# Optimization experiments

Measured on AMD Instinct MI355X. Metric: run time of the kernel, lower is better.

## Reference

```python
import jax, jax.numpy as jnp
import numpy as np

B, C, L, F = 4096, 1000, 32, 64


def _l2norm(x, eps=1e-12):
    # torch F.normalize: x / max(||x||_2, eps)
    n = jnp.sqrt(jnp.sum(x * x, axis=-1, keepdims=True))
    return x / jnp.maximum(n, eps)


def setup_inputs() -> dict:
    key = jax.random.key(0)
    k1, k2, k3 = jax.random.split(key, 3)
    pe = jax.random.normal(k1, (B, L, F), dtype=jnp.float32)
    cm = jax.random.uniform(k2, (B,), dtype=jnp.float32)
    class_signatures = jax.random.normal(k3, (C, L, F), dtype=jnp.float32) * 0.1
    cantor_prototypes = jnp.linspace(0.0, 1.0, C, dtype=jnp.float32)
    level_resonance = jnp.ones((C, L), dtype=jnp.float32) / L
    return {
        "pe_levels": pe,
        "cantor_measures": cm,
        "class_signatures": class_signatures,
        "cantor_prototypes": cantor_prototypes,
        "level_resonance": level_resonance,
    }


def reference(pe_levels, cantor_measures, class_signatures, cantor_prototypes, level_resonance):
    eps = 1e-6
    # --- triadic compatibility ---
    pe_norm = _l2norm(pe_levels)                     # [B,L,F]
    sig_norm = _l2norm(class_signatures)             # [C,L,F]
    sims = jnp.einsum('blf,clf->bcl', pe_norm, sig_norm)
    sims = (sims + 1.0) * 0.5                        # [B,C,L]
    resonance = jax.nn.softmax(level_resonance, axis=-1)  # [C,L]
    triadic = jnp.sum(sims * resonance[None, :, :], axis=-1)  # [B,C]
    # --- self-similarity pattern (vectorized over level pairs) ---
    a = pe_levels[:, :-1, :]                         # [B,L-1,F]
    b = pe_levels[:, 1:, :]
    cos_eps = 1e-8
    dot = jnp.sum(a * b, axis=-1)
    na = jnp.maximum(jnp.sqrt(jnp.sum(a * a, axis=-1)), cos_eps)
    nb = jnp.maximum(jnp.sqrt(jnp.sum(b * b, axis=-1)), cos_eps)
    self_sim = (dot / (na * nb) + 1.0) * 0.5         # [B,L-1]
    expected = jax.nn.sigmoid(level_resonance[:, :-1] - level_resonance[:, 1:])  # [C,L-1]
    pattern_diff = jnp.abs(self_sim[:, None, :] - expected[None, :, :])  # [B,C,L-1]
    self_sim_compat = jnp.clip(1.0 - jnp.mean(pattern_diff, axis=-1), 0.0, 1.0)  # [B,C]
    # --- cantor compatibility ---
    d = jnp.abs(cantor_measures[:, None] - cantor_prototypes[None, :])
    cantor_compat = jnp.exp(-(d * d) / 0.1) + 1e-8   # [B,C]
    # --- hierarchical compatibility ---
    split = L // 2
    early = _l2norm(jnp.mean(pe_levels[:, :split, :], axis=1))          # [B,F]
    late = _l2norm(jnp.mean(pe_levels[:, split:, :], axis=1))
    early_t = _l2norm(jnp.mean(class_signatures[:, :split, :], axis=1))  # [C,F]
    late_t = _l2norm(jnp.mean(class_signatures[:, split:, :], axis=1))
    early_c = (early @ early_t.T + 1.0) * 0.5
    late_c = (late @ late_t.T + 1.0) * 0.5
    hier = (early_c + late_c) * 0.5                  # [B,C]
    # --- geometric mean of four clamped terms ---
    t = jnp.clip(triadic, eps, 1.0)
    s = jnp.clip(self_sim_compat, eps, 1.0)
    c = jnp.clip(cantor_compat, eps, 1.0)
    h = jnp.clip(hier, eps, 1.0)
    return (t * s * c * h) ** 0.25
```

## Files before the change

kernel.cpp:

```cpp
#include <hip/hip_runtime.h>
#include <hip/hip_bf16.h>
#include <hip/hip_fp8.h>

typedef float f32x4 __attribute__((ext_vector_type(4)));
typedef short bf16x8 __attribute__((ext_vector_type(8)));

#define B_DIM 4096
#define C_DIM 1000
#define CP 1024
#define K1 2048
#define EPS 1e-6f

__device__ __forceinline__ float wsum(float v) {
#pragma unroll
  for (int o = 32; o > 0; o >>= 1) v += __shfl_xor(v, o, 64);
  return v;
}
__device__ __forceinline__ float wmax(float v) {
#pragma unroll
  for (int o = 32; o > 0; o >>= 1) v = fmaxf(v, __shfl_xor(v, o, 64));
  return v;
}

__device__ __forceinline__ void load_lds16(const void* g, void* l) {
  __builtin_amdgcn_global_load_lds(
      (const __attribute__((address_space(1))) unsigned int*)g,
      (__attribute__((address_space(3))) unsigned int*)l, 16, 0, 0);
}

__global__ void prep_all(const float* __restrict__ sig,
                         const float* __restrict__ lr,
                         const float* __restrict__ pe,
                         __hip_fp8_e4m3* __restrict__ wsig,
                         float* __restrict__ expd,
                         __hip_bfloat16* __restrict__ elc,
                         __hip_fp8_e4m3* __restrict__ pen,
                         float* __restrict__ ssb,
                         __hip_bfloat16* __restrict__ elb) {
  __shared__ float LW[4][2304];
  __shared__ float AUX[4][32];
  const int w = threadIdx.x >> 6;
  const int t = threadIdx.x & 63;
  const int unit = blockIdx.x * 4 + w;
  const bool isClass = unit < CP;
  const int c = unit;
  const int b = unit - CP;
  const bool pad = isClass && (c >= C_DIM);
  const float* src = isClass ? (sig + (size_t)c * K1) : (pe + (size_t)b * K1);

#pragma unroll
  for (int i = 0; i < 8; ++i) {
    int o = i * 256 + t * 4;
    f32x4 v = {0.f, 0.f, 0.f, 0.f};
    if (!pad) v = *(const f32x4*)(src + o);
    *(f32x4*)&LW[w][(o >> 6) * 72 + (o & 63)] = v;
  }
  __syncthreads();

  if (isClass) {
    float lv = (t < 32 && !pad) ? lr[c * 32 + t] : -3.0e38f;
    float mx = wmax(lv);
    float ev = (t < 32 && !pad) ? expf(lv - mx) : 0.f;
    float sden = wsum(ev);
    float res = pad ? 0.f : ev / sden;
    float lvn = __shfl_down(lv, 1, 64);
    if (t < 31) {
      expd[c * 32 + t] = pad ? 0.f : 1.f / (1.f + expf(-(lv - lvn)));
    } else if (t == 31) {
      expd[c * 32 + 31] = 0.f;
    }
    if (t < 32) {
      f32x4 sq = {0.f, 0.f, 0.f, 0.f};
#pragma unroll
      for (int i = 0; i < 16; ++i) {
        f32x4 v = *(const f32x4*)&LW[w][t * 72 + i * 4];
        sq += v * v;
      }
      float s = sq[0] + sq[1] + sq[2] + sq[3];
      float inv = 1.f / fmaxf(sqrtf(s), 1e-12f);
      AUX[w][t] = inv * res * 32.f;
    }
  } else {
    if (t < 32) {
      f32x4 sq = {0.f, 0.f, 0.f, 0.f}, dt = {0.f, 0.f, 0.f, 0.f};
      const int tn = (t < 31) ? t + 1 : t;
#pragma unroll
      for (int i = 0; i < 16; ++i) {
        f32x4 v = *(const f32x4*)&LW[w][t * 72 + i * 4];
        f32x4 vn = *(const f32x4*)&LW[w][tn * 72 + i * 4];
        sq += v * v;
        dt += v * vn;
      }
      float s = sq[0] + sq[1] + sq[2] + sq[3];
      float d = dt[0] + dt[1] + dt[2] + dt[3];
      float nrm = sqrtf(s);
      AUX[w][t] = 1.f / fmaxf(nrm, 1e-12f);
      float nn = __shfl_down(nrm, 1, 64);
      if (t < 31)
        ssb[(size_t)b * 32 + t] =
            (d / (fmaxf(nrm, 1e-8f) * fmaxf(nn, 1e-8f)) + 1.f) * 0.5f;
      else
        ssb[(size_t)b * 32 + 31] = 0.f;
    }
  }
  __syncthreads();

  __hip_fp8_e4m3* dst = isClass ? (wsig + (size_t)c * K1) : (pen + (size_t)b * K1);
  float es = 0.f, ls = 0.f;
#pragma unroll
  for (int l = 0; l < 32; ++l) {
    float v = LW[w][l * 72 + t];
    float m = AUX[w][l];
    dst[l * 64 + t] = __hip_fp8_e4m3(v * m);
    if (l < 16) es += v; else ls += v;
  }
  es *= (1.f / 16.f);
  ls *= (1.f / 16.f);
  float en = fmaxf(sqrtf(wsum(es * es)), 1e-12f);
  float ln2 = fmaxf(sqrtf(wsum(ls * ls)), 1e-12f);
  __hip_bfloat16* el = isClass ? (elc + (size_t)c * 128) : (elb + (size_t)b * 128);
  el[t] = __float2bfloat16(es / en);
  el[64 + t] = __float2bfloat16(ls / ln2);
}

__global__ __launch_bounds__(256, 2)
void basin_main(const unsigned char* __restrict__ pen,
                const unsigned char* __restrict__ wsig,
                const __hip_bfloat16* __restrict__ elb,
                const __hip_bfloat16* __restrict__ elc,
                const float* __restrict__ ssb,
                const float* __restrict__ expd,
                const float* __restrict__ cm,
                const float* __restrict__ proto,
                float* __restrict__ out) {
  __shared__ __align__(16) char smem[32768];
  const int t = threadIdx.x;
  const int lane = t & 63;
  const int w = t >> 6;
  const int wm = w >> 1, wn = w & 1;
  const int brow = blockIdx.x * 64;
  const int bcol = blockIdx.y * 64;
  const int srow = t >> 3;
  const int schunk = t & 7;
  const int sel = ((schunk ^ (srow & 7)) << 4);
  const int l15 = lane & 15;
  const int gq = lane >> 4;

  const int rowAb = (wm * 32 + l15) << 7;
  const int rowBb = ((wn * 32 + l15) << 7) + 8192;
  int xg8[4];
#pragma unroll
  for (int kk = 0; kk < 4; ++kk)
    xg8[kk] = ((((kk * 2 + (gq >> 1)) ^ (l15 & 7)) << 4) | ((gq & 1) << 3));
  int xgh[2];
#pragma unroll
  for (int kk = 0; kk < 2; ++kk) xgh[kk] = (((kk * 4 + gq) ^ (l15 & 7)) << 4);

  f32x4 acc1[2][2] = {};
  f32x4 acc2[2][2] = {};

#define STAGE_T(kt, BI)                                                                   \
  do {                                                                                    \
    _Pragma("unroll") for (int i = 0; i < 2; ++i) {                                       \
      load_lds16(pen + (size_t)(brow + i * 32 + srow) * K1 + (kt) * 128 + sel,            \
                 smem + (BI) * 16384 + i * 4096 + t * 16);                                \
      load_lds16(wsig + (size_t)(bcol + i * 32 + srow) * K1 + (kt) * 128 + sel,           \
                 smem + (BI) * 16384 + 8192 + i * 4096 + t * 16);                         \
    }                                                                                     \
  } while (0)

#define STAGE_H(s, BI)                                                                    \
  do {                                                                                    \
    _Pragma("unroll") for (int i = 0; i < 2; ++i) {                                       \
      load_lds16(elb + (size_t)(brow + i * 32 + srow) * 128 + (s) * 64 + (sel >> 1),      \
                 smem + (BI) * 16384 + i * 4096 + t * 16);                                \
      load_lds16(elc + (size_t)(bcol + i * 32 + srow) * 128 + (s) * 64 + (sel >> 1),      \
                 smem + (BI) * 16384 + 8192 + i * 4096 + t * 16);                         \
    }                                                                                     \
  } while (0)

#define COMPUTE(ACC, BI)                                                                  \
  do {                                                                                    \
    _Pragma("unroll") for (int kk = 0; kk < 4; ++kk) {                                    \
      long af[2], bg[2];                                                                  \
      _Pragma("unroll") for (int m = 0; m < 2; ++m)                                       \
          af[m] = *(const long*)(smem + (BI) * 16384 + rowAb + m * 2048 + xg8[kk]);       \
      _Pragma("unroll") for (int n = 0; n < 2; ++n)                                       \
          bg[n] = *(const long*)(smem + (BI) * 16384 + rowBb + n * 2048 + xg8[kk]);       \
      _Pragma("unroll") for (int m = 0; m < 2; ++m)                                       \
        _Pragma("unroll") for (int n = 0; n < 2; ++n)                                     \
          ACC[m][n] = __builtin_amdgcn_mfma_f32_16x16x32_fp8_fp8(af[m], bg[n], ACC[m][n], 0, 0, 0); \
    }                                                                                     \
  } while (0)

#define COMPUTE_H(ACC, BI)                                                                \
  do {                                                                                    \
    _Pragma("unroll") for (int kk = 0; kk < 2; ++kk) {                                    \
      bf16x8 af[2], bg[2];                                                                \
      _Pragma("unroll") for (int m = 0; m < 2; ++m)                                       \
          af[m] = *(const bf16x8*)(smem + (BI) * 16384 + rowAb + m * 2048 + xgh[kk]);     \
      _Pragma("unroll") for (int n = 0; n < 2; ++n)                                       \
          bg[n] = *(const bf16x8*)(smem + (BI) * 16384 + rowBb + n * 2048 + xgh[kk]);     \
      _Pragma("unroll") for (int m = 0; m < 2; ++m)                                       \
        _Pragma("unroll") for (int n = 0; n < 2; ++n)                                     \
          ACC[m][n] = __builtin_amdgcn_mfma_f32_16x16x32_bf16(af[m], bg[n], ACC[m][n], 0, 0, 0); \
    }                                                                                     \
  } while (0)

#define VMW(N) asm volatile("s_waitcnt vmcnt(" #N ")" ::: "memory")
#define BAR()                    \
  __builtin_amdgcn_s_barrier();  \
  __builtin_amdgcn_sched_barrier(0)

#define KSTEP(kt, BI, OTHER)                                                              \
  do {                                                                                    \
    VMW(0);                                                                               \
    BAR();                                                                                \
    if ((kt) + 1 < 16) STAGE_T((kt) + 1, OTHER);                                          \
    COMPUTE(acc1, BI);                                                                    \
  } while (0)

  STAGE_T(0, 0);
  for (int kt = 0; kt < 16; kt += 2) {
    KSTEP(kt, 0, 1);
    KSTEP(kt + 1, 1, 0);
  }
  __syncthreads();

  STAGE_H(0, 0);
  STAGE_H(1, 1);
  VMW(4); BAR();
  COMPUTE_H(acc2, 0);
  VMW(0); BAR();
  COMPUTE_H(acc2, 1);
  __syncthreads();

  float* ss_l = (float*)smem;
  float* ex_l = (float*)(smem + 9216);
  float* cm_l = (float*)(smem + 18432);
  float* pr_l = (float*)(smem + 18688);
  for (int i = t; i < 2048; i += 256) {
    int r = i >> 5, l = i & 31;
    ss_l[r * 36 + l] = ssb[(size_t)(brow + r) * 32 + l];
    ex_l[r * 36 + l] = expd[(size_t)(bcol + r) * 32 + l];
  }
  if (t < 64) cm_l[t] = cm[brow + t];
  else if (t < 128) pr_l[t - 64] = (bcol + t - 64 < C_DIM) ? proto[bcol + t - 64] : 0.f;
  __syncthreads();

  const int col0 = wn * 32 + l15;
  const int row0 = wm * 32 + (gq << 2);
#pragma unroll
  for (int m = 0; m < 2; ++m) {
    float ssum[4][2];
#pragma unroll
    for (int j = 0; j < 4; ++j)
#pragma unroll
      for (int n = 0; n < 2; ++n) ssum[j][n] = 0.f;
#pragma unroll
    for (int l4 = 0; l4 < 32; l4 += 4) {
      f32x4 evv[2], sv[4];
#pragma unroll
      for (int n = 0; n < 2; ++n)
        evv[n] = *(const f32x4*)&ex_l[(col0 + n * 16) * 36 + l4];
#pragma unroll
      for (int j = 0; j < 4; ++j)
        sv[j] = *(const f32x4*)&ss_l[(row0 + m * 16 + j) * 36 + l4];
#pragma unroll
      for (int j = 0; j < 4; ++j)
#pragma unroll
        for (int n = 0; n < 2; ++n) {
          ssum[j][n] += fabsf(sv[j][0] - evv[n][0]) + fabsf(sv[j][1] - evv[n][1]) +
                        fabsf(sv[j][2] - evv[n][2]) + fabsf(sv[j][3] - evv[n][3]);
        }
    }
#pragma unroll
    for (int j = 0; j < 4; ++j) {
      int rloc = row0 + m * 16 + j;
      float cmv = cm_l[rloc];
#pragma unroll
      for (int n = 0; n < 2; ++n) {
        int cloc = col0 + n * 16;
        int cg = bcol + cloc;
        float tria = fminf(fmaxf(0.5f + acc1[m][n][j] * 0.015625f, EPS), 1.0f);
        float hier = fminf(fmaxf(0.5f + 0.25f * acc2[m][n][j], EPS), 1.0f);
        float sc = fminf(fmaxf(1.0f - ssum[j][n] * (1.0f / 31.0f), EPS), 1.0f);
        float d = cmv - pr_l[cloc];
        float cc = __expf(d * d * -10.0f) + 1e-8f;
        cc = fminf(fmaxf(cc, EPS), 1.0f);
        float p = tria * sc * cc * hier;
        if (cg < C_DIM)
          out[(size_t)(brow + rloc) * C_DIM + cg] = sqrtf(sqrtf(p));
      }
    }
  }
}

extern "C" void kernel_launch(void* const* d_in, const int* in_sizes, int n_in,
                              void* d_out, int out_size, void* d_ws, size_t ws_size,
                              hipStream_t stream) {
  (void)in_sizes; (void)n_in; (void)out_size; (void)ws_size;
  const float* pe = (const float*)d_in[0];
  const float* cm = (const float*)d_in[1];
  const float* sig = (const float*)d_in[2];
  const float* proto = (const float*)d_in[3];
  const float* lr = (const float*)d_in[4];
  float* out = (float*)d_out;
  char* ws = (char*)d_ws;

  __hip_fp8_e4m3* wsig = (__hip_fp8_e4m3*)(ws);
  __hip_fp8_e4m3* pen = (__hip_fp8_e4m3*)(ws + 2097152);
  __hip_bfloat16* elb = (__hip_bfloat16*)(ws + 10485760);
  __hip_bfloat16* elc = (__hip_bfloat16*)(ws + 11534336);
  float* ssb = (float*)(ws + 11796480);
  float* expd = (float*)(ws + 12320768);

  prep_all<<<(CP + B_DIM) / 4, 256, 0, stream>>>(sig, lr, pe, wsig, expd, elc, pen, ssb, elb);
  dim3 grid(B_DIM / 64, CP / 64);
  basin_main<<<grid, 256, 0, stream>>>((const unsigned char*)pen, (const unsigned char*)wsig,
                                       elb, elc, ssb, expd, cm, proto, out);
}
```

Baseline: 58.87 us.

## Widen fp8 LDS reads, overlap hier staging with last GEMM step, swap grid order

The fp8 fragment loads now use 16-byte LDS reads, each feeding two MFMAs, which halves the number of LDS read instructions. The last triadic k-step is peeled so the hierarchical bf16 tiles are staged while the final fp8 compute runs, removing a full sync and a serialized load phase. The grid axes are swapped so neighbouring blocks share the same B rows and walk the C columns, which changes L2 reuse. The K-split across MFMAs changes (each lane now holds contiguous 16 bytes), but because A and B are permuted the same way the dot product stays correct.

```diff
diff --git a/kernel.cpp b/kernel.cpp
--- a/kernel.cpp
+++ b/kernel.cpp
@@ -4,6 +4,7 @@
 
 typedef float f32x4 __attribute__((ext_vector_type(4)));
 typedef short bf16x8 __attribute__((ext_vector_type(8)));
+typedef long longx2 __attribute__((ext_vector_type(2)));
 
 #define B_DIM 4096
 #define C_DIM 1000
@@ -138,8 +139,8 @@
   const int lane = t & 63;
   const int w = t >> 6;
   const int wm = w >> 1, wn = w & 1;
-  const int brow = blockIdx.x * 64;
-  const int bcol = blockIdx.y * 64;
+  const int brow = blockIdx.y * 64;
+  const int bcol = blockIdx.x * 64;
   const int srow = t >> 3;
   const int schunk = t & 7;
   const int sel = ((schunk ^ (srow & 7)) << 4);
@@ -148,10 +149,9 @@
 
   const int rowAb = (wm * 32 + l15) << 7;
   const int rowBb = ((wn * 32 + l15) << 7) + 8192;
-  int xg8[4];
-#pragma unroll
-  for (int kk = 0; kk < 4; ++kk)
-    xg8[kk] = ((((kk * 2 + (gq >> 1)) ^ (l15 & 7)) << 4) | ((gq & 1) << 3));
+  int xc[2];
+  xc[0] = ((gq ^ (l15 & 7)) << 4);
+  xc[1] = (((gq + 4) ^ (l15 & 7)) << 4);
   int xgh[2];
 #pragma unroll
   for (int kk = 0; kk < 2; ++kk) xgh[kk] = (((kk * 4 + gq) ^ (l15 & 7)) << 4);
@@ -181,15 +181,17 @@
 
 #define COMPUTE(ACC, BI)                                                                  \
   do {                                                                                    \
-    _Pragma("unroll") for (int kk = 0; kk < 4; ++kk) {                                    \
-      long af[2], bg[2];                                                                  \
-      _Pragma("unroll") for (int m = 0; m < 2; ++m)                                       \
-          af[m] = *(const long*)(smem + (BI) * 16384 + rowAb + m * 2048 + xg8[kk]);       \
-      _Pragma("unroll") for (int n = 0; n < 2; ++n)                                       \
-          bg[n] = *(const long*)(smem + (BI) * 16384 + rowBb + n * 2048 + xg8[kk]);       \
-      _Pragma("unroll") for (int m = 0; m < 2; ++m)                                       \
-        _Pragma("unroll") for (int n = 0; n < 2; ++n)                                     \
-          ACC[m][n] = __builtin_amdgcn_mfma_f32_16x16x32_fp8_fp8(af[m], bg[n], ACC[m][n], 0, 0, 0); \
+    _Pragma("unroll") for (int c = 0; c < 2; ++c) {                                       \
+      longx2 ar[2], br[2];                                                                \
+      _Pragma("unroll") for (int m = 0; m < 2; ++m) {                                     \
+        ar[m] = *(const longx2*)(smem + (BI) * 16384 + rowAb + m * 2048 + xc[c]);         \
+        br[m] = *(const longx2*)(smem + (BI) * 16384 + rowBb + m * 2048 + xc[c]);         \
+      }                                                                                   \
+      _Pragma("unroll") for (int h = 0; h < 2; ++h)                                       \
+        _Pragma("unroll") for (int m = 0; m < 2; ++m)                                     \
+          _Pragma("unroll") for (int n = 0; n < 2; ++n)                                   \
+            ACC[m][n] = __builtin_amdgcn_mfma_f32_16x16x32_fp8_fp8(                       \
+                ar[m][h], br[n][h], ACC[m][n], 0, 0, 0);                                  \
     }                                                                                     \
   } while (0)
 
@@ -221,18 +223,14 @@
   } while (0)
 
   STAGE_T(0, 0);
-  for (int kt = 0; kt < 16; kt += 2) {
+  for (int kt = 0; kt < 14; kt += 2) {
     KSTEP(kt, 0, 1);
     KSTEP(kt + 1, 1, 0);
   }
-  __syncthreads();
-
-  STAGE_H(0, 0);
-  STAGE_H(1, 1);
-  VMW(4); BAR();
-  COMPUTE_H(acc2, 0);
-  VMW(0); BAR();
-  COMPUTE_H(acc2, 1);
+  KSTEP(14, 0, 1);
+  VMW(0); BAR(); STAGE_H(0, 0); COMPUTE(acc1, 1);
+  VMW(0); BAR(); STAGE_H(1, 1); COMPUTE_H(acc2, 0);
+  VMW(0); BAR(); COMPUTE_H(acc2, 1);
   __syncthreads();
 
   float* ss_l = (float*)smem;
@@ -316,7 +314,7 @@
   float* expd = (float*)(ws + 12320768);
 
   prep_all<<<(CP + B_DIM) / 4, 256, 0, stream>>>(sig, lr, pe, wsig, expd, elc, pen, ssb, elb);
-  dim3 grid(B_DIM / 64, CP / 64);
+  dim3 grid(CP / 64, B_DIM / 64);
   basin_main<<<grid, 256, 0, stream>>>((const unsigned char*)pen, (const unsigned char*)wsig,
                                        elb, elc, ssb, expd, cm, proto, out);
 }
```

Measured after the change: 60.37 us. +2.5%, slower.

## Load fp8 GEMM operands straight into registers, skipping LDS staging

Applied to the files above, without the earlier changes.

The main fp8 MFMA loop no longer stages A and B tiles through shared memory with barriers. Each lane now reads its 16-byte K slices directly from global memory into registers, with two register buffers so the next loads overlap the current MFMAs. This removes the LDS round-trip and the per-step waitcnt and barriers. In exchange, waves sharing a row redundantly fetch the same data from global/L2, access is less coalesced, and register pressure rises, which may hurt occupancy.

```diff
diff --git a/kernel.cpp b/kernel.cpp
--- a/kernel.cpp
+++ b/kernel.cpp
@@ -4,6 +4,7 @@
 
 typedef float f32x4 __attribute__((ext_vector_type(4)));
 typedef short bf16x8 __attribute__((ext_vector_type(8)));
+typedef long longx2 __attribute__((ext_vector_type(2)));
 
 #define B_DIM 4096
 #define C_DIM 1000
@@ -140,34 +141,66 @@
   const int wm = w >> 1, wn = w & 1;
   const int brow = blockIdx.x * 64;
   const int bcol = blockIdx.y * 64;
-  const int srow = t >> 3;
-  const int schunk = t & 7;
-  const int sel = ((schunk ^ (srow & 7)) << 4);
   const int l15 = lane & 15;
   const int gq = lane >> 4;
-
+  const int go = gq * 16;
+
+  const unsigned char* aP0 = pen + (size_t)(brow + wm * 32 + l15) * K1;
+  const unsigned char* aP1 = pen + (size_t)(brow + wm * 32 + 16 + l15) * K1;
+  const unsigned char* bP0 = wsig + (size_t)(bcol + wn * 32 + l15) * K1;
+  const unsigned char* bP1 = wsig + (size_t)(bcol + wn * 32 + 16 + l15) * K1;
+
+  f32x4 acc1[2][2] = {};
+  f32x4 acc2[2][2] = {};
+
+#define MFMA8(A, B, ACC) \
+  ACC = __builtin_amdgcn_mfma_f32_16x16x32_fp8_fp8(A, B, ACC, 0, 0, 0)
+
+#define DECL_BUF(S) longx2 S##a00, S##a01, S##a10, S##a11, S##b00, S##b01, S##b10, S##b11
+#define LOAD_STEP(S, kt)                                   \
+  do {                                                     \
+    int _o = (kt) * 128 + go;                              \
+    S##a00 = *(const longx2*)(aP0 + _o);                   \
+    S##a01 = *(const longx2*)(aP0 + _o + 64);              \
+    S##a10 = *(const longx2*)(aP1 + _o);                   \
+    S##a11 = *(const longx2*)(aP1 + _o + 64);              \
+    S##b00 = *(const longx2*)(bP0 + _o);                   \
+    S##b01 = *(const longx2*)(bP0 + _o + 64);              \
+    S##b10 = *(const longx2*)(bP1 + _o);                   \
+    S##b11 = *(const longx2*)(bP1 + _o + 64);              \
+  } while (0)
+#define MFMA_STEP(S)                                       \
+  do {                                                     \
+    _Pragma("unroll") for (int h = 0; h < 2; ++h) {        \
+      MFMA8(S##a00[h], S##b00[h], acc1[0][0]);             \
+      MFMA8(S##a00[h], S##b10[h], acc1[0][1]);             \
+      MFMA8(S##a10[h], S##b00[h], acc1[1][0]);             \
+      MFMA8(S##a10[h], S##b10[h], acc1[1][1]);             \
+      MFMA8(S##a01[h], S##b01[h], acc1[0][0]);             \
+      MFMA8(S##a01[h], S##b11[h], acc1[0][1]);             \
+      MFMA8(S##a11[h], S##b01[h], acc1[1][0]);             \
+      MFMA8(S##a11[h], S##b11[h], acc1[1][1]);             \
+    }                                                      \
+  } while (0)
+
+  DECL_BUF(P);
+  DECL_BUF(Q);
+  LOAD_STEP(P, 0);
+  LOAD_STEP(Q, 1);
+  for (int kt = 0; kt < 16; kt += 2) {
+    MFMA_STEP(P);
+    if (kt + 2 < 16) LOAD_STEP(P, kt + 2);
+    MFMA_STEP(Q);
+    if (kt + 3 < 16) LOAD_STEP(Q, kt + 3);
+  }
+
+  const int srow = t >> 3;
+  const int sel = (((t & 7) ^ (srow & 7)) << 4);
   const int rowAb = (wm * 32 + l15) << 7;
   const int rowBb = ((wn * 32 + l15) << 7) + 8192;
-  int xg8[4];
-#pragma unroll
-  for (int kk = 0; kk < 4; ++kk)
-    xg8[kk] = ((((kk * 2 + (gq >> 1)) ^ (l15 & 7)) << 4) | ((gq & 1) << 3));
   int xgh[2];
 #pragma unroll
   for (int kk = 0; kk < 2; ++kk) xgh[kk] = (((kk * 4 + gq) ^ (l15 & 7)) << 4);
-
-  f32x4 acc1[2][2] = {};
-  f32x4 acc2[2][2] = {};
-
-#define STAGE_T(kt, BI)                                                                   \
-  do {                                                                                    \
-    _Pragma("unroll") for (int i = 0; i < 2; ++i) {                                       \
-      load_lds16(pen + (size_t)(brow + i * 32 + srow) * K1 + (kt) * 128 + sel,            \
-                 smem + (BI) * 16384 + i * 4096 + t * 16);                                \
-      load_lds16(wsig + (size_t)(bcol + i * 32 + srow) * K1 + (kt) * 128 + sel,           \
-                 smem + (BI) * 16384 + 8192 + i * 4096 + t * 16);                         \
-    }                                                                                     \
-  } while (0)
 
 #define STAGE_H(s, BI)                                                                    \
   do {                                                                                    \
@@ -176,20 +209,6 @@
                  smem + (BI) * 16384 + i * 4096 + t * 16);                                \
       load_lds16(elc + (size_t)(bcol + i * 32 + srow) * 128 + (s) * 64 + (sel >> 1),      \
                  smem + (BI) * 16384 + 8192 + i * 4096 + t * 16);                         \
-    }                                                                                     \
-  } while (0)
-
-#define COMPUTE(ACC, BI)                                                                  \
-  do {                                                                                    \
-    _Pragma("unroll") for (int kk = 0; kk < 4; ++kk) {                                    \
-      long af[2], bg[2];                                                                  \
-      _Pragma("unroll") for (int m = 0; m < 2; ++m)                                       \
-          af[m] = *(const long*)(smem + (BI) * 16384 + rowAb + m * 2048 + xg8[kk]);       \
-      _Pragma("unroll") for (int n = 0; n < 2; ++n)                                       \
-          bg[n] = *(const long*)(smem + (BI) * 16384 + rowBb + n * 2048 + xg8[kk]);       \
-      _Pragma("unroll") for (int m = 0; m < 2; ++m)                                       \
-        _Pragma("unroll") for (int n = 0; n < 2; ++n)                                     \
-          ACC[m][n] = __builtin_amdgcn_mfma_f32_16x16x32_fp8_fp8(af[m], bg[n], ACC[m][n], 0, 0, 0); \
     }                                                                                     \
   } while (0)
 
@@ -212,21 +231,6 @@
   __builtin_amdgcn_s_barrier();  \
   __builtin_amdgcn_sched_barrier(0)
 
-#define KSTEP(kt, BI, OTHER)                                                              \
-  do {                                                                                    \
-    VMW(0);                                                                               \
-    BAR();                                                                                \
-    if ((kt) + 1 < 16) STAGE_T((kt) + 1, OTHER);                                          \
-    COMPUTE(acc1, BI);                                                                    \
-  } while (0)
-
-  STAGE_T(0, 0);
-  for (int kt = 0; kt < 16; kt += 2) {
-    KSTEP(kt, 0, 1);
-    KSTEP(kt + 1, 1, 0);
-  }
-  __syncthreads();
-
   STAGE_H(0, 0);
   STAGE_H(1, 1);
   VMW(4); BAR();
```

New measurement: 96.17 us. 1.63x slower.
